# Kernel optimization log

Hardware: AMD Instinct MI355X
Metric: run time of the kernel (lower is better)

The kernel has to match this reference:

```python
import jax, jax.numpy as jnp
import numpy as np

B, S, D, H = 8, 1024, 1024, 16
DH = D // H  # head dim = 64 (extend_head=False split)
EPS = 1e-5


def setup_inputs() -> dict:
    key = jax.random.key(0)
    ks = jax.random.split(key, 9)
    s = 0.02
    return {
        "query": jax.random.normal(ks[0], (B, S, D), jnp.float32),
        "key":   jax.random.normal(ks[1], (B, S, D), jnp.float32),
        "value": jax.random.normal(ks[2], (B, S, D), jnp.float32),
        "mask":  jnp.ones((B, S), jnp.bool_),
        # Linear weights stored [in, out] (torch uses [out, in]; math identical)
        "Wq": jax.random.normal(ks[3], (D, D), jnp.float32) * s,
        "bq": jnp.zeros((D,), jnp.float32),
        "Wk": jax.random.normal(ks[4], (D, D), jnp.float32) * s,
        "bk": jnp.zeros((D,), jnp.float32),
        "Wv": jax.random.normal(ks[5], (D, D), jnp.float32) * s,
        "bv": jnp.zeros((D,), jnp.float32),
        # BatchNorm1d affine params
        "gamma": jnp.ones((D,), jnp.float32),
        "beta":  jnp.zeros((D,), jnp.float32),
    }


def _split_heads(x):
    # torch: cat(x.split(DH, -1), 0) -> head-major stacking [H*B, S, DH]
    return x.reshape(B, S, H, DH).transpose(2, 0, 1, 3)  # [H,B,S,DH]


def reference(query, key, value, mask, Wq, bq, Wk, bk, Wv, bv, gamma, beta):
    q = query @ Wq + bq   # [B,S,D]
    k = key   @ Wk + bk
    v = value @ Wv + bv

    qh = _split_heads(q)  # [H,B,S,DH]
    kh = _split_heads(k)
    vh = _split_heads(v)

    # NOTE: source builds an additive mask but never applies it to the
    # scores -> faithful reference uses UNMASKED softmax.
    scores = jnp.einsum('hbqd,hbkd->hbqk', qh, kh) / np.sqrt(DH).astype(np.float32)
    weights = jax.nn.softmax(scores, axis=-1)          # [H,B,S,S]
    out = jnp.einsum('hbqk,hbkd->hbqd', weights, vh)   # [H,B,S,DH]

    # cat(split(out, B, 0), -1): re-concatenate heads on feature dim
    out = out.transpose(1, 2, 0, 3).reshape(B, S, D)

    # row-gather by boolean mask (all-ones -> static shape [B*S, D])
    out = out.reshape(-1, D)[mask.reshape(-1)]

    # BatchNorm1d (training-mode batch stats, biased var) + SiLU
    mean = out.mean(axis=0)
    var = jnp.mean(jnp.square(out - mean), axis=0)
    out = (out - mean) / jnp.sqrt(var + EPS) * gamma + beta
    return jax.nn.silu(out)
```

## Files before the change

### kernel.cpp

```cpp
#include <hip/hip_runtime.h>
#include <hip/hip_bf16.h>
#include <cstdint>
#include <cstddef>

#define B_ 8
#define S_ 1024
#define D_ 1024
#define H_ 16
#define DH_ 64

using f32x4   = __attribute__((ext_vector_type(4))) float;
using f32x16  = __attribute__((ext_vector_type(16))) float;
using float4v = __attribute__((ext_vector_type(4))) float;
using bf16x8  = __attribute__((ext_vector_type(8))) short;
using ushort8 = __attribute__((ext_vector_type(8))) unsigned short;
using uint2v  = __attribute__((ext_vector_type(2))) unsigned int;

__device__ __forceinline__ unsigned short f2bf(float f) {
    union { float f; unsigned u; } v; v.f = f;
    unsigned r = v.u + 0x7FFF + ((v.u >> 16) & 1);
    return (unsigned short)(r >> 16);
}
__device__ __forceinline__ float bf2f(unsigned short b) {
    union { unsigned u; float f; } v; v.u = ((unsigned)b) << 16;
    return v.f;
}

#if __has_builtin(__builtin_amdgcn_exp2f)
__device__ __forceinline__ float fexp2(float x) { return __builtin_amdgcn_exp2f(x); }
#else
__device__ __forceinline__ float fexp2(float x) { return __expf(x * 0.69314718056f); }
#endif

__device__ __forceinline__ unsigned cvtpk_bf16(float lo, float hi) {
    unsigned r;
    asm("v_cvt_pk_bf16_f32 %0, %1, %2" : "=v"(r) : "v"(lo), "v"(hi));
    return r;
}

__device__ __forceinline__ void gl_lds16(const unsigned short* g, unsigned short* l) {
    __builtin_amdgcn_global_load_lds(
        (const __attribute__((address_space(1))) unsigned int*)g,
        (__attribute__((address_space(3))) unsigned int*)l,
        16, 0, 0);
}

__global__ __launch_bounds__(256) void prep_kernel(
    const float* __restrict__ Wq, const float* __restrict__ Wk, const float* __restrict__ Wv,
    const float* __restrict__ Xq, const float* __restrict__ Xk, const float* __restrict__ Xv,
    unsigned short* __restrict__ Wt,
    unsigned short* __restrict__ Bq, unsigned short* __restrict__ Bk, unsigned short* __restrict__ Bv,
    float* __restrict__ gsum)
{
    __shared__ float tile[32][33];
    int bid = blockIdx.x;
    int t = threadIdx.x;

    if (bid == 0) {
#pragma unroll
        for (int j = 0; j < 8; ++j) gsum[t + 256 * j] = 0.f;
    }

    if (bid < 3072) {
        int z = bid >> 10, rc = bid & 1023;
        const float* W = (z == 0) ? Wq : (z == 1) ? Wk : Wv;
        unsigned short* Y = Wt + (size_t)z * 1048576;
        int tx = t & 31, ty = t >> 5;
        int r0 = (rc >> 5) * 32, c0 = (rc & 31) * 32;
#pragma unroll
        for (int j = 0; j < 4; ++j) {
            int r = ty + j * 8;
            tile[r][tx] = W[(size_t)(r0 + r) * D_ + c0 + tx];
        }
        __syncthreads();
#pragma unroll
        for (int j = 0; j < 4; ++j) {
            int r = ty + j * 8;
            Y[(size_t)(c0 + r) * D_ + r0 + tx] = f2bf(tile[tx][r]);
        }
    } else {
        int cid = bid - 3072;
        int which = cid >> 12;
        int blk = cid & 4095;
        const float* X = (which == 0) ? Xq : (which == 1) ? Xk : Xv;
        unsigned short* Y = (which == 0) ? Bq : (which == 1) ? Bk : Bv;
        size_t idx = ((size_t)blk * 256 + t) * 8;
        float4v v0 = *reinterpret_cast<const float4v*>(X + idx);
        float4v v1 = *reinterpret_cast<const float4v*>(X + idx + 4);
        ushort8 o;
#pragma unroll
        for (int j = 0; j < 4; ++j) { o[j] = f2bf(v0[j]); o[j + 4] = f2bf(v1[j]); }
        *reinterpret_cast<ushort8*>(Y + idx) = o;
    }
}

__global__ __launch_bounds__(512, 2) void qkv_gemm8(
    const unsigned short* __restrict__ Xbq, const unsigned short* __restrict__ Xbk, const unsigned short* __restrict__ Xbv,
    const unsigned short* __restrict__ Wts,
    const float* __restrict__ bq, const float* __restrict__ bk, const float* __restrict__ bv,
    unsigned short* __restrict__ Qh, unsigned short* __restrict__ Kf, unsigned short* __restrict__ Vf)
{
    extern __shared__ unsigned short smem[];
    unsigned short* lA = smem;
    unsigned short* lB = smem + 32768;

    int bid = blockIdx.x;
    int L = (bid & 7) * 48 + (bid >> 3);
    int mode = L >> 7;
    int rem = L & 127;
    int bm = rem >> 2;
    int bn = rem & 3;

    const unsigned short* Xb = (mode == 0) ? Xbq : (mode == 1) ? Xbk : Xbv;
    const unsigned short* Wt = Wts + (size_t)mode * 1048576;
    const float* bias = (mode == 0) ? bq : (mode == 1) ? bk : bv;

    int t = threadIdx.x;
    int m0 = bm * 256, n0 = bn * 256;
    int wid = t >> 6, lane = t & 63;
    int wr = wid >> 2, wc = wid & 3;
    int lr = lane & 15, lg = lane >> 4;

    int srow = t >> 3;
    int scol = (((t & 7) ^ (srow & 7))) * 8;
    const unsigned short* Asrc = Xb + (size_t)(m0 + srow) * D_ + scol;
    const unsigned short* Bsrc = Wt + (size_t)(n0 + srow) * D_ + scol;
    unsigned short* lAdst = lA + t * 8;
    unsigned short* lBdst = lB + t * 8;

#define STAGE_A(buf, pass, kt) gl_lds16(Asrc + (size_t)(pass) * 64 * D_ + (kt) * 64, lAdst + (buf) * 16384 + (pass) * 4096)
#define STAGE_B(buf, pass, kt) gl_lds16(Bsrc + (size_t)(pass) * 64 * D_ + (kt) * 64, lBdst + (buf) * 16384 + (pass) * 4096)

#define READ_A(dst, base, half)                                                      \
    _Pragma("unroll") for (int m_ = 0; m_ < 4; ++m_) {                               \
        int R_ = wr * 128 + (half) * 64 + m_ * 16 + lr;                              \
        _Pragma("unroll") for (int ks_ = 0; ks_ < 2; ++ks_) {                        \
            int pc_ = ((ks_ * 4 + lg) ^ (R_ & 7)) * 8;                               \
            dst[m_][ks_] = *reinterpret_cast<const bf16x8*>((base) + R_ * 64 + pc_); \
        }                                                                            \
    }
#define READ_B2(base, nb)                                                            \
    _Pragma("unroll") for (int n_ = 0; n_ < 2; ++n_) {                               \
        int R_ = wc * 64 + ((nb) + n_) * 16 + lr;                                    \
        _Pragma("unroll") for (int ks_ = 0; ks_ < 2; ++ks_) {                        \
            int pc_ = ((ks_ * 4 + lg) ^ (R_ & 7)) * 8;                               \
            b[(nb) + n_][ks_] = *reinterpret_cast<const bf16x8*>((base) + R_ * 64 + pc_); \
        }                                                                            \
    }
#define MFMA_BLK(A_, MB, NB)                                                         \
    _Pragma("unroll") for (int m_ = 0; m_ < 4; ++m_)                                 \
        _Pragma("unroll") for (int n_ = 0; n_ < 2; ++n_)                             \
            _Pragma("unroll") for (int ks_ = 0; ks_ < 2; ++ks_)                      \
                acc[(MB) + m_][(NB) + n_] = __builtin_amdgcn_mfma_f32_16x16x32_bf16( \
                    A_[m_][ks_], b[(NB) + n_][ks_], acc[(MB) + m_][(NB) + n_], 0, 0, 0);

#define BAR1() do { __builtin_amdgcn_s_barrier();                                    \
                    asm volatile("s_waitcnt lgkmcnt(0)" ::: "memory");               \
                    __builtin_amdgcn_sched_barrier(0);                               \
                    __builtin_amdgcn_s_setprio(1); } while (0)
#define BAR2() do { __builtin_amdgcn_s_setprio(0);                                   \
                    __builtin_amdgcn_s_barrier();                                    \
                    __builtin_amdgcn_sched_barrier(0); } while (0)

    f32x4 acc[8][4] = {};
    bf16x8 a[4][2], a2[4][2], b[4][2];

    STAGE_A(0, 0, 0); STAGE_A(0, 1, 0); STAGE_A(0, 2, 0); STAGE_A(0, 3, 0);
    STAGE_B(0, 0, 0); STAGE_B(0, 1, 0); STAGE_B(0, 2, 0); STAGE_B(0, 3, 0);
    STAGE_A(1, 0, 1); STAGE_A(1, 1, 1);
    asm volatile("s_waitcnt vmcnt(2)" ::: "memory");
    __builtin_amdgcn_s_barrier();
    __builtin_amdgcn_sched_barrier(0);

#pragma unroll 1
    for (int i = 0; i < 8; ++i) {
        int c1 = 2 * i + 1, nt0 = 2 * i + 2, nt1 = 2 * i + 3;
        bool g0 = (nt0 < 16), g1 = (nt1 < 16);
        const unsigned short* A0p = lA;
        const unsigned short* B0p = lB;
        const unsigned short* A1p = lA + 16384;
        const unsigned short* B1p = lB + 16384;

        READ_A(a, A0p, 0); READ_B2(B0p, 0);
        STAGE_A(1, 2, c1); STAGE_A(1, 3, c1);
        BAR1(); MFMA_BLK(a, 0, 0); BAR2();

        READ_B2(B0p, 2);
        STAGE_B(1, 0, c1); STAGE_B(1, 1, c1);
        BAR1(); MFMA_BLK(a, 0, 2); BAR2();

        READ_A(a2, A0p, 1);
        STAGE_B(1, 2, c1); STAGE_B(1, 3, c1);
        BAR1(); MFMA_BLK(a2, 4, 0); BAR2();

        if (g0) { STAGE_A(0, 0, nt0); STAGE_A(0, 1, nt0); }
        BAR1(); MFMA_BLK(a2, 4, 2);
        __builtin_amdgcn_s_setprio(0);
        if (g0) asm volatile("s_waitcnt vmcnt(2)" ::: "memory");
        else    asm volatile("s_waitcnt vmcnt(0)" ::: "memory");
        __builtin_amdgcn_s_barrier();
        __builtin_amdgcn_sched_barrier(0);

        READ_A(a, A1p, 0); READ_B2(B1p, 0);
        if (g0) { STAGE_A(0, 2, nt0); STAGE_A(0, 3, nt0); }
        BAR1(); MFMA_BLK(a, 0, 0); BAR2();

        READ_B2(B1p, 2);
        if (g0) { STAGE_B(0, 0, nt0); STAGE_B(0, 1, nt0); }
        BAR1(); MFMA_BLK(a, 0, 2); BAR2();

        READ_A(a2, A1p, 1);
        if (g0) { STAGE_B(0, 2, nt0); STAGE_B(0, 3, nt0); }
        BAR1(); MFMA_BLK(a2, 4, 0); BAR2();

        if (g1) { STAGE_A(1, 0, nt1); STAGE_A(1, 1, nt1); }
        BAR1(); MFMA_BLK(a2, 4, 2);
        __builtin_amdgcn_s_setprio(0);
        if (g1) asm volatile("s_waitcnt vmcnt(2)" ::: "memory");
        else    asm volatile("s_waitcnt vmcnt(0)" ::: "memory");
        __builtin_amdgcn_s_barrier();
        __builtin_amdgcn_sched_barrier(0);
    }
#undef BAR1
#undef BAR2
#undef MFMA_BLK
#undef READ_A
#undef READ_B2
#undef STAGE_A
#undef STAGE_B

#pragma unroll
    for (int am = 0; am < 8; ++am) {
#pragma unroll
        for (int an = 0; an < 4; ++an) {
            int col = n0 + wc * 64 + an * 16 + lr;
            int h = col >> 6, d = col & 63;
            float bval = bias[col];
#pragma unroll
            for (int r = 0; r < 4; ++r) {
                int row = m0 + wr * 128 + am * 16 + lg * 4 + r;
                int bb = row >> 10, s = row & 1023;
                int inst = h * B_ + bb;
                float v = acc[am][an][r] + bval;
                if (mode == 0) {
                    Qh[((size_t)inst * S_ + s) * DH_ + d] = f2bf(v * 0.18033688f);
                } else if (mode == 1) {
                    int kt2 = s >> 6, n_ = (s >> 5) & 1, cl = s & 31;
                    int dk = d >> 4, hi2 = (d >> 3) & 1, j = d & 7;
                    size_t off = ((((size_t)inst * 16 + kt2) * 2 + n_) * 4 + dk) * 512
                               + (size_t)(hi2 * 32 + cl) * 8 + j;
                    Kf[off] = f2bf(v);
                } else {
                    int kt2 = s >> 6, ks2 = (s >> 4) & 3, hi2 = (s >> 3) & 1, j = s & 7;
                    int nd = d >> 5, cl = d & 31;
                    size_t off = ((((size_t)inst * 16 + kt2) * 2 + nd) * 4 + ks2) * 512
                               + (size_t)(hi2 * 32 + cl) * 8 + j;
                    Vf[off] = f2bf(v);
                }
            }
        }
    }
}

__global__ __launch_bounds__(512, 2) void attn_kernel(
    const unsigned short* __restrict__ Qh,
    const unsigned short* __restrict__ Kf,
    const unsigned short* __restrict__ Vf,
    unsigned short* __restrict__ O,
    float* __restrict__ gsum, float* __restrict__ gsq)
{
    __shared__ unsigned short ldsK[2][4096];
    __shared__ unsigned short ldsV[2][4096];
    __shared__ float part[8][64][4];

    int inst = blockIdx.x;
    int h = inst >> 3, bb = inst & 7;
    int t = threadIdx.x, wid = t >> 6, lane = t & 63;
    int cl = lane & 31, hi = lane >> 5;
    int q0 = (blockIdx.y * 8 + wid) * 32;

    const unsigned short* Qb = Qh + (size_t)inst * S_ * DH_ + (size_t)(q0 + cl) * DH_ + hi * 8;
    const unsigned short* Kt = Kf + (size_t)inst * 65536;
    const unsigned short* Vt = Vf + (size_t)inst * 65536;

    bf16x8 qf[4];
#pragma unroll
    for (int dk = 0; dk < 4; ++dk)
        qf[dk] = *reinterpret_cast<const bf16x8*>(Qb + dk * 16);

#define STAGE_KV(buf, kt) do {                                              \
        gl_lds16(Kt + (size_t)(kt) * 4096 + t * 8, &ldsK[buf][t * 8]);      \
        gl_lds16(Vt + (size_t)(kt) * 4096 + t * 8, &ldsV[buf][t * 8]);      \
    } while (0)

    STAGE_KV(0, 0);
    STAGE_KV(1, 1);

    f32x16 o0 = {}, o1 = {};
    float li = 0.f;

#pragma unroll 1
    for (int kt = 0; kt < S_ / 64; ++kt) {
        int buf = kt & 1;
        asm volatile("s_waitcnt vmcnt(2)" ::: "memory");
        __builtin_amdgcn_s_barrier();
        __builtin_amdgcn_sched_barrier(0);

        const unsigned short* kb = &ldsK[buf][0] + lane * 8;
        const unsigned short* vp = &ldsV[buf][0] + lane * 8;

        bf16x8 ka[2][4];
#pragma unroll
        for (int n = 0; n < 2; ++n)
#pragma unroll
            for (int dk = 0; dk < 4; ++dk)
                ka[n][dk] = *reinterpret_cast<const bf16x8*>(kb + (n * 4 + dk) * 512);

        bf16x8 vb0[4], vb1[4];
#pragma unroll
        for (int ks = 0; ks < 4; ++ks) {
            vb0[ks] = *reinterpret_cast<const bf16x8*>(vp + ks * 512);
            vb1[ks] = *reinterpret_cast<const bf16x8*>(vp + (4 + ks) * 512);
        }

        f32x16 s0 = {}, s1 = {};
        __builtin_amdgcn_s_setprio(1);
#pragma unroll
        for (int dk = 0; dk < 4; ++dk)
            s0 = __builtin_amdgcn_mfma_f32_32x32x16_bf16(ka[0][dk], qf[dk], s0, 0, 0, 0);
#pragma unroll
        for (int dk = 0; dk < 4; ++dk)
            s1 = __builtin_amdgcn_mfma_f32_32x32x16_bf16(ka[1][dk], qf[dk], s1, 0, 0, 0);
        __builtin_amdgcn_s_setprio(0);

        float p0[16], p1[16];
#pragma unroll
        for (int i = 0; i < 16; ++i) { p0[i] = fexp2(s0[i]); p1[i] = fexp2(s1[i]); }
        float ts[16];
#pragma unroll
        for (int i = 0; i < 16; ++i) ts[i] = p0[i] + p1[i];
#pragma unroll
        for (int st = 8; st > 0; st >>= 1)
#pragma unroll
            for (int i = 0; i < st; ++i) ts[i] += ts[i + st];
        li += ts[0] + __shfl_xor(ts[0], 32, 64);

        unsigned w[16];
#pragma unroll
        for (int i = 0; i < 8; ++i) w[i]     = cvtpk_bf16(p0[2 * i], p0[2 * i + 1]);
#pragma unroll
        for (int i = 0; i < 8; ++i) w[8 + i] = cvtpk_bf16(p1[2 * i], p1[2 * i + 1]);

        bf16x8 pa[4];
#pragma unroll
        for (int g = 0; g < 4; ++g) {
            uint2v ra = __builtin_amdgcn_permlane32_swap(w[4 * g + 0], w[4 * g + 2], false, false);
            uint2v rb = __builtin_amdgcn_permlane32_swap(w[4 * g + 1], w[4 * g + 3], false, false);
            union { unsigned u[4]; bf16x8 v; } cv;
            cv.u[0] = ra[0]; cv.u[1] = rb[0]; cv.u[2] = ra[1]; cv.u[3] = rb[1];
            pa[g] = cv.v;
        }

        __builtin_amdgcn_s_setprio(1);
#pragma unroll
        for (int g = 0; g < 4; ++g) {
            o0 = __builtin_amdgcn_mfma_f32_32x32x16_bf16(pa[g], vb0[g], o0, 0, 0, 0);
            o1 = __builtin_amdgcn_mfma_f32_32x32x16_bf16(pa[g], vb1[g], o1, 0, 0, 0);
        }
        __builtin_amdgcn_s_setprio(0);

        asm volatile("s_waitcnt lgkmcnt(0)" ::: "memory");
        __builtin_amdgcn_s_barrier();
        __builtin_amdgcn_sched_barrier(0);
        if (kt + 2 < S_ / 64) STAGE_KV(buf, kt + 2);
    }
#undef STAGE_KV

    float rli = 1.0f / li;
    float sa = 0.f, qa = 0.f, sb = 0.f, qb2 = 0.f;
#pragma unroll
    for (int r = 0; r < 16; ++r) {
        int qr = (r & 3) + 8 * (r >> 2) + 4 * hi;
        float inv = __shfl(rli, qr, 64);
        int s = q0 + qr;
        size_t base = ((size_t)bb * S_ + s) * D_ + h * DH_;
        float y0 = o0[r] * inv, y1 = o1[r] * inv;
        O[base + cl]      = f2bf(y0);
        O[base + 32 + cl] = f2bf(y1);
        sa += y0; qa += y0 * y0; sb += y1; qb2 += y1 * y1;
    }
    part[wid][lane][0] = sa; part[wid][lane][1] = qa;
    part[wid][lane][2] = sb; part[wid][lane][3] = qb2;
    __syncthreads();
    if (t < 128) {
        int cl2 = t >> 2, st = t & 3;
        float acc = 0.f;
#pragma unroll
        for (int w2 = 0; w2 < 8; ++w2)
            acc += part[w2][cl2][st] + part[w2][cl2 + 32][st];
        int col = h * 64 + cl2 + ((st >= 2) ? 32 : 0);
        float* tgt = (st & 1) ? gsq : gsum;
        atomicAdd(&tgt[col], acc);
    }
}

__global__ __launch_bounds__(256) void bn_apply(const unsigned short* __restrict__ O,
                                                const float* __restrict__ gsum,
                                                const float* __restrict__ gsq,
                                                const float* __restrict__ gamma,
                                                const float* __restrict__ beta,
                                                float* __restrict__ out) {
    const float invN = 1.f / 8192.f;
    size_t idx = ((size_t)blockIdx.x * 256 + threadIdx.x) * 8;
    int col0 = (int)(idx & 1023);
    ushort8 v = *reinterpret_cast<const ushort8*>(O + idx);
#pragma unroll
    for (int j = 0; j < 8; ++j) {
        int c = col0 + j;
        float mean = gsum[c] * invN;
        float var = gsq[c] * invN - mean * mean;
        float rstd = rsqrtf(var + 1e-5f);
        float x = bf2f(v[j]);
        float y = (x - mean) * rstd * gamma[c] + beta[c];
        out[idx + j] = y / (1.f + __expf(-y));
    }
}

extern "C" void kernel_launch(void* const* d_in, const int* in_sizes, int n_in,
                              void* d_out, int out_size, void* d_ws, size_t ws_size,
                              hipStream_t stream) {
    const float* query = (const float*)d_in[0];
    const float* key   = (const float*)d_in[1];
    const float* value = (const float*)d_in[2];
    const float* Wq = (const float*)d_in[4];
    const float* bq = (const float*)d_in[5];
    const float* Wk = (const float*)d_in[6];
    const float* bk = (const float*)d_in[7];
    const float* Wv = (const float*)d_in[8];
    const float* bv = (const float*)d_in[9];
    const float* gamma = (const float*)d_in[10];
    const float* beta  = (const float*)d_in[11];

    char* w = (char*)d_ws;
    unsigned short* Wt  = (unsigned short*)w;
    unsigned short* Qh  = (unsigned short*)(w + (6u << 20));
    unsigned short* Kf  = Qh + 8388608;
    unsigned short* Vf  = Kf + 8388608;
    unsigned short* Xbq = Vf + 8388608;
    unsigned short* Xbk = Xbq + 8388608;
    unsigned short* Xbv = Xbk + 8388608;
    unsigned short* O   = Xbq;
    float* gsum = (float*)(Xbv + 8388608);
    float* gsq  = gsum + 1024;

    prep_kernel<<<dim3(15360), 256, 0, stream>>>(Wq, Wk, Wv, query, key, value,
                                                 Wt, Xbq, Xbk, Xbv, gsum);

    hipFuncSetAttribute(reinterpret_cast<const void*>(&qkv_gemm8),
                        hipFuncAttributeMaxDynamicSharedMemorySize, 131072);
    qkv_gemm8<<<dim3(384), 512, 131072, stream>>>(Xbq, Xbk, Xbv, Wt,
                                                  bq, bk, bv, Qh, Kf, Vf);

    attn_kernel<<<dim3(128, 4), 512, 0, stream>>>(Qh, Kf, Vf, O, gsum, gsq);

    bn_apply<<<4096, 256, 0, stream>>>(O, gsum, gsq, gamma, beta, (float*)d_out);
}
```

Baseline: 166.0 us.

## Shrink QKV GEMM tile to 256x128 and double grid size

The QKV projection GEMM moves from 256x256 to 256x128 output tiles. The grid grows from 384 to 768 blocks and LDS per block drops from 128KB to 96KB. The staging and MFMA pipeline is rebuilt around the smaller B tile, with fewer accumulators and changed global-to-LDS staging order and waitcnts. The aim is better occupancy and wave balance across CUs, at the cost of lower arithmetic intensity and more A-matrix reloads.

```diff
diff --git a/kernel.cpp b/kernel.cpp
--- a/kernel.cpp
+++ b/kernel.cpp
@@ -105,18 +105,18 @@
     unsigned short* lB = smem + 32768;
 
     int bid = blockIdx.x;
-    int L = (bid & 7) * 48 + (bid >> 3);
-    int mode = L >> 7;
-    int rem = L & 127;
-    int bm = rem >> 2;
-    int bn = rem & 3;
+    int L = (bid & 7) * 96 + (bid >> 3);
+    int mode = L >> 8;
+    int rem = L & 255;
+    int bm = rem >> 3;
+    int bn = rem & 7;
 
     const unsigned short* Xb = (mode == 0) ? Xbq : (mode == 1) ? Xbk : Xbv;
     const unsigned short* Wt = Wts + (size_t)mode * 1048576;
     const float* bias = (mode == 0) ? bq : (mode == 1) ? bk : bv;
 
     int t = threadIdx.x;
-    int m0 = bm * 256, n0 = bn * 256;
+    int m0 = bm * 256, n0 = bn * 128;
     int wid = t >> 6, lane = t & 63;
     int wr = wid >> 2, wc = wid & 3;
     int lr = lane & 15, lg = lane >> 4;
@@ -129,7 +129,7 @@
     unsigned short* lBdst = lB + t * 8;
 
 #define STAGE_A(buf, pass, kt) gl_lds16(Asrc + (size_t)(pass) * 64 * D_ + (kt) * 64, lAdst + (buf) * 16384 + (pass) * 4096)
-#define STAGE_B(buf, pass, kt) gl_lds16(Bsrc + (size_t)(pass) * 64 * D_ + (kt) * 64, lBdst + (buf) * 16384 + (pass) * 4096)
+#define STAGE_B(buf, pass, kt) gl_lds16(Bsrc + (size_t)(pass) * 64 * D_ + (kt) * 64, lBdst + (buf) * 8192 + (pass) * 4096)
 
 #define READ_A(dst, base, half)                                                      \
     _Pragma("unroll") for (int m_ = 0; m_ < 4; ++m_) {                               \
@@ -139,20 +139,20 @@
             dst[m_][ks_] = *reinterpret_cast<const bf16x8*>((base) + R_ * 64 + pc_); \
         }                                                                            \
     }
-#define READ_B2(base, nb)                                                            \
+#define READ_B(base)                                                                 \
     _Pragma("unroll") for (int n_ = 0; n_ < 2; ++n_) {                               \
-        int R_ = wc * 64 + ((nb) + n_) * 16 + lr;                                    \
+        int R_ = wc * 32 + n_ * 16 + lr;                                             \
         _Pragma("unroll") for (int ks_ = 0; ks_ < 2; ++ks_) {                        \
             int pc_ = ((ks_ * 4 + lg) ^ (R_ & 7)) * 8;                               \
-            b[(nb) + n_][ks_] = *reinterpret_cast<const bf16x8*>((base) + R_ * 64 + pc_); \
+            b[n_][ks_] = *reinterpret_cast<const bf16x8*>((base) + R_ * 64 + pc_);   \
         }                                                                            \
     }
-#define MFMA_BLK(A_, MB, NB)                                                         \
+#define MFMA_BLK(A_, MB)                                                             \
     _Pragma("unroll") for (int m_ = 0; m_ < 4; ++m_)                                 \
         _Pragma("unroll") for (int n_ = 0; n_ < 2; ++n_)                             \
             _Pragma("unroll") for (int ks_ = 0; ks_ < 2; ++ks_)                      \
-                acc[(MB) + m_][(NB) + n_] = __builtin_amdgcn_mfma_f32_16x16x32_bf16( \
-                    A_[m_][ks_], b[(NB) + n_][ks_], acc[(MB) + m_][(NB) + n_], 0, 0, 0);
+                acc[(MB) + m_][n_] = __builtin_amdgcn_mfma_f32_16x16x32_bf16(        \
+                    A_[m_][ks_], b[n_][ks_], acc[(MB) + m_][n_], 0, 0, 0);
 
 #define BAR1() do { __builtin_amdgcn_s_barrier();                                    \
                     asm volatile("s_waitcnt lgkmcnt(0)" ::: "memory");               \
@@ -162,13 +162,13 @@
                     __builtin_amdgcn_s_barrier();                                    \
                     __builtin_amdgcn_sched_barrier(0); } while (0)
 
-    f32x4 acc[8][4] = {};
-    bf16x8 a[4][2], a2[4][2], b[4][2];
+    f32x4 acc[8][2] = {};
+    bf16x8 a[4][2], a2[4][2], b[2][2];
 
     STAGE_A(0, 0, 0); STAGE_A(0, 1, 0); STAGE_A(0, 2, 0); STAGE_A(0, 3, 0);
-    STAGE_B(0, 0, 0); STAGE_B(0, 1, 0); STAGE_B(0, 2, 0); STAGE_B(0, 3, 0);
-    STAGE_A(1, 0, 1); STAGE_A(1, 1, 1);
-    asm volatile("s_waitcnt vmcnt(2)" ::: "memory");
+    STAGE_B(0, 0, 0); STAGE_B(0, 1, 0);
+    STAGE_A(1, 0, 1); STAGE_A(1, 1, 1); STAGE_A(1, 2, 1);
+    asm volatile("s_waitcnt vmcnt(3)" ::: "memory");
     __builtin_amdgcn_s_barrier();
     __builtin_amdgcn_sched_barrier(0);
 
@@ -179,45 +179,37 @@
         const unsigned short* A0p = lA;
         const unsigned short* B0p = lB;
         const unsigned short* A1p = lA + 16384;
-        const unsigned short* B1p = lB + 16384;
-
-        READ_A(a, A0p, 0); READ_B2(B0p, 0);
-        STAGE_A(1, 2, c1); STAGE_A(1, 3, c1);
-        BAR1(); MFMA_BLK(a, 0, 0); BAR2();
-
-        READ_B2(B0p, 2);
-        STAGE_B(1, 0, c1); STAGE_B(1, 1, c1);
-        BAR1(); MFMA_BLK(a, 0, 2); BAR2();
+        const unsigned short* B1p = lB + 8192;
+
+        READ_A(a, A0p, 0); READ_B(B0p);
+        STAGE_A(1, 3, c1); STAGE_B(1, 0, c1); STAGE_B(1, 1, c1);
+        BAR1(); MFMA_BLK(a, 0); BAR2();
 
         READ_A(a2, A0p, 1);
-        STAGE_B(1, 2, c1); STAGE_B(1, 3, c1);
-        BAR1(); MFMA_BLK(a2, 4, 0); BAR2();
-
-        if (g0) { STAGE_A(0, 0, nt0); STAGE_A(0, 1, nt0); }
-        BAR1(); MFMA_BLK(a2, 4, 2);
+        BAR1(); MFMA_BLK(a2, 4);
         __builtin_amdgcn_s_setprio(0);
-        if (g0) asm volatile("s_waitcnt vmcnt(2)" ::: "memory");
-        else    asm volatile("s_waitcnt vmcnt(0)" ::: "memory");
+        if (g0) {
+            STAGE_A(0, 0, nt0); STAGE_A(0, 1, nt0); STAGE_A(0, 2, nt0);
+            asm volatile("s_waitcnt vmcnt(3)" ::: "memory");
+        } else {
+            asm volatile("s_waitcnt vmcnt(0)" ::: "memory");
+        }
         __builtin_amdgcn_s_barrier();
         __builtin_amdgcn_sched_barrier(0);
 
-        READ_A(a, A1p, 0); READ_B2(B1p, 0);
-        if (g0) { STAGE_A(0, 2, nt0); STAGE_A(0, 3, nt0); }
-        BAR1(); MFMA_BLK(a, 0, 0); BAR2();
-
-        READ_B2(B1p, 2);
-        if (g0) { STAGE_B(0, 0, nt0); STAGE_B(0, 1, nt0); }
-        BAR1(); MFMA_BLK(a, 0, 2); BAR2();
+        READ_A(a, A1p, 0); READ_B(B1p);
+        if (g0) { STAGE_A(0, 3, nt0); STAGE_B(0, 0, nt0); STAGE_B(0, 1, nt0); }
+        BAR1(); MFMA_BLK(a, 0); BAR2();
 
         READ_A(a2, A1p, 1);
-        if (g0) { STAGE_B(0, 2, nt0); STAGE_B(0, 3, nt0); }
-        BAR1(); MFMA_BLK(a2, 4, 0); BAR2();
-
-        if (g1) { STAGE_A(1, 0, nt1); STAGE_A(1, 1, nt1); }
-        BAR1(); MFMA_BLK(a2, 4, 2);
+        BAR1(); MFMA_BLK(a2, 4);
         __builtin_amdgcn_s_setprio(0);
-        if (g1) asm volatile("s_waitcnt vmcnt(2)" ::: "memory");
-        else    asm volatile("s_waitcnt vmcnt(0)" ::: "memory");
+        if (g1) {
+            STAGE_A(1, 0, nt1); STAGE_A(1, 1, nt1); STAGE_A(1, 2, nt1);
+            asm volatile("s_waitcnt vmcnt(3)" ::: "memory");
+        } else {
+            asm volatile("s_waitcnt vmcnt(0)" ::: "memory");
+        }
         __builtin_amdgcn_s_barrier();
         __builtin_amdgcn_sched_barrier(0);
     }
@@ -225,15 +217,15 @@
 #undef BAR2
 #undef MFMA_BLK
 #undef READ_A
-#undef READ_B2
+#undef READ_B
 #undef STAGE_A
 #undef STAGE_B
 
 #pragma unroll
     for (int am = 0; am < 8; ++am) {
 #pragma unroll
-        for (int an = 0; an < 4; ++an) {
-            int col = n0 + wc * 64 + an * 16 + lr;
+        for (int an = 0; an < 2; ++an) {
+            int col = n0 + wc * 32 + an * 16 + lr;
             int h = col >> 6, d = col & 63;
             float bval = bias[col];
 #pragma unroll
@@ -457,9 +449,9 @@
                                                  Wt, Xbq, Xbk, Xbv, gsum);
 
     hipFuncSetAttribute(reinterpret_cast<const void*>(&qkv_gemm8),
-                        hipFuncAttributeMaxDynamicSharedMemorySize, 131072);
-    qkv_gemm8<<<dim3(384), 512, 131072, stream>>>(Xbq, Xbk, Xbv, Wt,
-                                                  bq, bk, bv, Qh, Kf, Vf);
+                        hipFuncAttributeMaxDynamicSharedMemorySize, 98304);
+    qkv_gemm8<<<dim3(768), 512, 98304, stream>>>(Xbq, Xbk, Xbv, Wt,
+                                                 bq, bk, bv, Qh, Kf, Vf);
 
     attn_kernel<<<dim3(128, 4), 512, 0, stream>>>(Qh, Kf, Vf, O, gsum, gsq);
 
```

Result: faster. 155.3 us (-6.4%).
